# Optimization experiments

Measured on AMD Instinct MI355X. Metric: run time of the kernel, lower is better.

Reference implementation:

```python
import jax, jax.numpy as jnp
import numpy as np

N_NODES = 50000
N_EDGES = 800000
HIDDEN = 128
IN_DIM = 6
N_ACTIONS = 64
NUM_GRAPHS = 512


def setup_inputs() -> dict:
    key = jax.random.key(0)
    ks = jax.random.split(key, 9)
    x = jax.random.normal(ks[0], (N_NODES, IN_DIM), dtype=jnp.float32)
    edge_index = jax.random.randint(ks[1], (2, N_EDGES), 0, N_NODES, dtype=jnp.int64)
    batch_number = jnp.sort(jax.random.randint(ks[2], (N_NODES,), 0, NUM_GRAPHS, dtype=jnp.int64))
    s1 = 1.0 / np.sqrt(IN_DIM)
    s2 = 1.0 / np.sqrt(HIDDEN)
    w1 = jax.random.uniform(ks[3], (IN_DIM, HIDDEN), jnp.float32, -s1, s1)
    b1 = jnp.zeros((HIDDEN,), jnp.float32)
    wl = jax.random.uniform(ks[4], (HIDDEN, HIDDEN), jnp.float32, -s2, s2)
    bl = jax.random.uniform(ks[5], (HIDDEN,), jnp.float32, -s2, s2)
    w2 = jax.random.uniform(ks[6], (HIDDEN, N_ACTIONS), jnp.float32, -s2, s2)
    b2 = jax.random.uniform(ks[7], (N_ACTIONS,), jnp.float32, -s2, s2)
    return {"x": x, "edge_index": edge_index, "batch_number": batch_number,
            "w1": w1, "b1": b1, "wl": wl, "bl": bl, "w2": w2, "b2": b2}


def _gcn_conv(x, edge_index, w, b):
    # PyG GCNConv: add self-loops, symmetric D^-1/2 (A+I) D^-1/2, linear first.
    n = x.shape[0]
    loop = jnp.arange(n, dtype=edge_index.dtype)
    src = jnp.concatenate([edge_index[0], loop])
    dst = jnp.concatenate([edge_index[1], loop])
    deg = jax.ops.segment_sum(jnp.ones_like(dst, dtype=x.dtype), dst, num_segments=n)
    dinv = jax.lax.rsqrt(jnp.maximum(deg, 1.0))  # deg >= 1 from self-loops
    norm = dinv[src] * dinv[dst]                  # [E+N]
    h = x @ w                                     # [N, hidden]
    msg = h[src] * norm[:, None]                  # gather + edge-wise scale
    return jax.ops.segment_sum(msg, dst, num_segments=n) + b


def reference(x, edge_index, batch_number, w1, b1, wl, bl, w2, b2):
    h = jax.nn.relu(_gcn_conv(x, edge_index, w1, b1))          # [N, hidden]
    # scatter_mean over graphs in the batch
    gsum = jax.ops.segment_sum(h, batch_number, num_segments=NUM_GRAPHS)
    cnt = jax.ops.segment_sum(jnp.ones((h.shape[0],), h.dtype), batch_number,
                              num_segments=NUM_GRAPHS)
    g = gsum / jnp.maximum(cnt, 1.0)[:, None]                  # [G, hidden]
    g = jax.nn.relu(g @ wl + bl)
    logits = g @ w2 + b2                                       # [G, actions]
    return jax.nn.log_softmax(logits, axis=1)
```

## Files before the change

kernel.cpp:

```cpp
#include <hip/hip_runtime.h>
#include <math.h>

#define N_NODES 50000
#define N_EDGES 800000
#define HID     128
#define N_ACT   64
#define N_GRAPH 512
#define N6      (N_NODES * 6)

#define NWF    512
#define LOGW   9
#define WF     98
#define CB     8
#define DC     8
#define EPB    2048
#define PB     ((N_EDGES + EPB - 1) / EPB)
#define SEGCAP 64
#define SSH    6
#define MAXIT  7

#define MAXN  768

#define F_BUCKET 0
#define F_COUNTS (F_BUCKET + (WF * PB + 512) * SEGCAP)
#define F_GSTART (F_COUNTS + 38320)
#define F_DINV   (F_GSTART + 516)
#define F_XSPAD  (F_DINV + N_NODES)
#define F_DEGP   (F_XSPAD + N_NODES * 8)
#define F_SPART  (F_DEGP + DC * N_NODES)
#define F_TOTAL  (F_SPART + CB * N6)
#define NEED_BYTES ((size_t)F_TOTAL * 4)


__global__ __launch_bounds__(512) void k_place(const int* __restrict__ ei,
                                               int* __restrict__ bucket,
                                               int* __restrict__ counts) {
    __shared__ int lc[WF];
    int t = threadIdx.x;
    int b = blockIdx.x;
    if (t < WF) lc[t] = 0;
    __syncthreads();
    int e0 = b * EPB;
    int pk[4], wli[4];
#pragma unroll
    for (int i = 0; i < 4; ++i) {
        int e = e0 + i * 512 + t;
        wli[i] = -1;
        if (e < N_EDGES) {
            int src = ei[e], dst = ei[N_EDGES + e];
            int w = dst >> LOGW;
            int lp = atomicAdd(&lc[w], 1);
            pk[i] = ((dst - (w << LOGW)) << 16) | src;
            wli[i] = (w << 16) | lp;
        }
    }
    __syncthreads();
    if (t < WF) counts[t * PB + b] = min(lc[t], SEGCAP);
#pragma unroll
    for (int i = 0; i < 4; ++i) {
        if (wli[i] >= 0) {
            int w = wli[i] >> 16, lp = wli[i] & 0xffff;
            if (lp < SEGCAP) bucket[((w * PB + b) << SSH) + lp] = pk[i];
        }
    }
}

__global__ __launch_bounds__(512) void k_degp(const int* __restrict__ bucket,
                                              const int* __restrict__ counts,
                                              float* __restrict__ degp) {
    __shared__ float hist[NWF];
    __shared__ int scnt[64];
    int w = blockIdx.x, c = blockIdx.y;
    int t = threadIdx.x;
    int nseg = (PB - 1 - c) / DC + 1;
    if (t < NWF) hist[t] = 0.0f;
    if (t < 64) scnt[t] = 0;
    __syncthreads();
    if (t < nseg) scnt[t] = counts[w * PB + c + DC * t];
    __syncthreads();
    int base = (w * PB + c) << SSH;
    int pk[MAXIT];
    bool val[MAXIT];
#pragma unroll
    for (int i = 0; i < MAXIT; ++i) {
        int s = t + i * 512;
        int j = s >> SSH, e = s & (SEGCAP - 1);
        val[i] = e < scnt[j];
        pk[i] = bucket[base + ((j * DC) << SSH) + e];
    }
#pragma unroll
    for (int i = 0; i < MAXIT; ++i)
        if (val[i]) atomicAdd(&hist[((unsigned)pk[i]) >> 16], 1.0f);
    __syncthreads();
    int nb = w * NWF;
    int lim = min(NWF, N_NODES - nb);
    if (t < lim) degp[c * N_NODES + nb + t] = hist[t];
}

__device__ __forceinline__ void mark_gstart(const int* __restrict__ batch, int m,
                                            int* __restrict__ gstart) {
    int bm = batch[m];
    if (m == 0) {
        for (int g = 0; g <= bm; ++g) gstart[g] = 0;
    } else {
        int bp = batch[m - 1];
        for (int g = bp + 1; g <= bm; ++g) gstart[g] = m;
    }
    if (m == N_NODES - 1) {
        for (int g = bm + 1; g <= N_GRAPH; ++g) gstart[g] = N_NODES;
    }
}

__global__ __launch_bounds__(256) void k_scale2(const float* __restrict__ degp,
                                                const float* __restrict__ x,
                                                const int* __restrict__ batch,
                                                float* __restrict__ dinv,
                                                float* __restrict__ xs_pad,
                                                int* __restrict__ gstart) {
    int n = blockIdx.x * 512 + 2 * threadIdx.x;
    if (n >= N_NODES) return;
    float d0 = 1.0f, d1 = 1.0f;
#pragma unroll
    for (int c = 0; c < DC; ++c) {
        d0 += degp[c * N_NODES + n];
        d1 += degp[c * N_NODES + n + 1];
    }
    float dv0 = rsqrtf(d0), dv1 = rsqrtf(d1);
    dinv[n] = dv0; dinv[n + 1] = dv1;
    const float4* xp = (const float4*)(x + (size_t)n * 6);
    float4 xa = xp[0], xb = xp[1], xc = xp[2];
    float4* op = (float4*)(xs_pad + (size_t)n * 8);
    op[0] = make_float4(xa.x * dv0, xa.y * dv0, xa.z * dv0, xa.w * dv0);
    op[1] = make_float4(xb.x * dv0, xb.y * dv0, 0.0f, 0.0f);
    op[2] = make_float4(xb.z * dv1, xb.w * dv1, xc.x * dv1, xc.y * dv1);
    op[3] = make_float4(xc.z * dv1, xc.w * dv1, 0.0f, 0.0f);
    mark_gstart(batch, n, gstart);
    mark_gstart(batch, n + 1, gstart);
}

__global__ __launch_bounds__(512) void k_feat(const int* __restrict__ bucket,
                                              const int* __restrict__ counts,
                                              const float* __restrict__ xs_pad,
                                              float* __restrict__ s_part) {
    __shared__ float h[NWF * 6];
    __shared__ int scnt[64];
    int w = blockIdx.x, c = blockIdx.y;
    int t = threadIdx.x;
    float4* h4 = (float4*)h;
    for (int i = t; i < NWF * 6 / 4; i += 512) h4[i] = make_float4(0, 0, 0, 0);
    if (t < 64) scnt[t] = 0;
    __syncthreads();
    int nseg = (PB - 1 - c) / CB + 1;
    if (t < nseg) scnt[t] = counts[w * PB + c + CB * t];
    __syncthreads();
    int base = (w * PB + c) << SSH;

    int pk[MAXIT];
    bool val[MAXIT];
#pragma unroll
    for (int i = 0; i < MAXIT; ++i) {
        int s = t + i * 512;
        int j = s >> SSH, e = s & (SEGCAP - 1);
        val[i] = e < scnt[j];
        pk[i] = bucket[base + ((j * CB) << SSH) + e];
    }
    float4 ga[MAXIT], gb[MAXIT];
#pragma unroll
    for (int i = 0; i < MAXIT; ++i) {
        const float4* q = (const float4*)(xs_pad + (size_t)(pk[i] & 0xffff) * 8);
        ga[i] = q[0]; gb[i] = q[1];
    }
#pragma unroll
    for (int i = 0; i < MAXIT; ++i) {
        if (val[i]) {
            float* hp = &h[(((unsigned)pk[i]) >> 16) * 6];
            atomicAdd(hp + 0, ga[i].x); atomicAdd(hp + 1, ga[i].y); atomicAdd(hp + 2, ga[i].z);
            atomicAdd(hp + 3, ga[i].w); atomicAdd(hp + 4, gb[i].x); atomicAdd(hp + 5, gb[i].y);
        }
    }
    __syncthreads();
    int gbase = w * NWF * 6;
    int lim = min(NWF * 6, N6 - gbase);
    float4* sp4 = (float4*)(s_part + (size_t)c * N6 + gbase);
    for (int i = t; i < lim / 4; i += 512) sp4[i] = h4[i];
}

__global__ __launch_bounds__(512) void k_nodehead(const float* __restrict__ s_part,
                                                  const float* __restrict__ xs_pad,
                                                  const float* __restrict__ dinv,
                                                  const int* __restrict__ gstart,
                                                  const float* __restrict__ w1,
                                                  const float* __restrict__ b1,
                                                  const float* __restrict__ wl,
                                                  const float* __restrict__ bl,
                                                  const float* __restrict__ w2,
                                                  const float* __restrict__ b2,
                                                  float* __restrict__ out) {
    __shared__ float sb[MAXN * 6];
    __shared__ float dvb[MAXN];
    __shared__ float sg[4 * HID];
    __shared__ float sg2[4 * HID];
    __shared__ int gb[5];
    int t = threadIdx.x;
    int g0 = blockIdx.x * 4;
    if (t < 5) gb[t] = gstart[g0 + t];
    __syncthreads();
    int ns = gb[0], ne = gb[4];
    int sub = t >> 7, f = t & (HID - 1);
    float w1r[6];
#pragma unroll
    for (int k = 0; k < 6; ++k) w1r[k] = w1[k * HID + f];
    float b1f = b1[f];
    float acc = 0.0f;

    for (int base = ns; base < ne; base += MAXN) {
        int cc = min(MAXN, ne - base);
        __syncthreads();
        {
            float2* sb2 = (float2*)sb;
            int nel = cc * 3;
            int g2 = base * 3;
            for (int i = t; i < nel; i += 512) {
                float2 v = make_float2(0.0f, 0.0f);
#pragma unroll
                for (int c = 0; c < CB; ++c) {
                    float2 p = ((const float2*)(s_part + (size_t)c * N6))[g2 + i];
                    v.x += p.x; v.y += p.y;
                }
                sb2[i] = v;
            }
        }
        for (int i = t; i < cc; i += 512) {
            int n = base + i;
            const float4* xp = (const float4*)(xs_pad + (size_t)n * 8);
            float4 a = xp[0], bq = xp[1];
            float* sp = &sb[i * 6];
            sp[0] += a.x; sp[1] += a.y; sp[2] += a.z;
            sp[3] += a.w; sp[4] += bq.x; sp[5] += bq.y;
            dvb[i] = dinv[n];
        }
        __syncthreads();
        int lo = max(gb[sub], base);
        int hi = min(gb[sub + 1], base + cc);
        for (int n = lo; n < hi; ++n) {
            int i = n - base;
            const float* sp = &sb[i * 6];
            float tv = 0.0f;
#pragma unroll
            for (int k = 0; k < 6; ++k) tv = fmaf(sp[k], w1r[k], tv);
            acc += fmaxf(fmaf(dvb[i], tv, b1f), 0.0f);
        }
    }

    int cnt = gb[sub + 1] - gb[sub];
    float ic = 1.0f / fmaxf((float)cnt, 1.0f);
    sg[sub * HID + f] = acc * ic;
    __syncthreads();

    float a2 = bl[f];
    for (int k = 0; k < HID; ++k) a2 = fmaf(sg[sub * HID + k], wl[k * HID + f], a2);
    sg2[sub * HID + f] = fmaxf(a2, 0.0f);
    __syncthreads();

    if (f < N_ACT) {
        float l = b2[f];
        for (int ff = 0; ff < HID; ++ff) l = fmaf(sg2[sub * HID + ff], w2[ff * N_ACT + f], l);
        float m = l;
#pragma unroll
        for (int off = 32; off > 0; off >>= 1) m = fmaxf(m, __shfl_xor(m, off));
        float e = expf(l - m);
        float ssum = e;
#pragma unroll
        for (int off = 32; off > 0; off >>= 1) ssum += __shfl_xor(ssum, off);
        out[(g0 + sub) * N_ACT + f] = l - m - logf(ssum);
    }
}


__global__ void k_init(float* __restrict__ deg, float* __restrict__ gsum,
                       float* __restrict__ cnt) {
    int i = blockIdx.x * blockDim.x + threadIdx.x;
    if (i < N_NODES) deg[i] = 1.0f;
    if (i < N_GRAPH * HID) gsum[i] = 0.0f;
    if (i < N_GRAPH) cnt[i] = 0.0f;
}

__global__ void k_deg(const int* __restrict__ ei, float* __restrict__ deg) {
    int e = blockIdx.x * blockDim.x + threadIdx.x;
    if (e < N_EDGES) atomicAdd(&deg[ei[N_EDGES + e]], 1.0f);
}

__global__ void k_scale(const float* __restrict__ x, const int* __restrict__ batch,
                        const float* __restrict__ deg, float* __restrict__ dinv,
                        float* __restrict__ xs, float* __restrict__ s,
                        float* __restrict__ cnt) {
    int n = blockIdx.x * blockDim.x + threadIdx.x;
    if (n >= N_NODES) return;
    float dv = rsqrtf(deg[n]);
    dinv[n] = dv;
#pragma unroll
    for (int k = 0; k < 6; ++k) {
        float v = x[n * 6 + k] * dv;
        xs[n * 6 + k] = v;
        s[n * 6 + k] = v;
    }
    atomicAdd(&cnt[batch[n]], 1.0f);
}

__global__ void k_scatter(const int* __restrict__ ei, const float* __restrict__ xs,
                          float* __restrict__ s) {
    int e = blockIdx.x * blockDim.x + threadIdx.x;
    if (e >= N_EDGES) return;
    int src = ei[e];
    int dst = ei[N_EDGES + e];
#pragma unroll
    for (int k = 0; k < 6; ++k)
        atomicAdd(&s[dst * 6 + k], xs[src * 6 + k]);
}

__global__ __launch_bounds__(256) void k_node(const float* __restrict__ s,
                                              const float* __restrict__ dinv,
                                              const int* __restrict__ batch,
                                              const float* __restrict__ w1,
                                              const float* __restrict__ b1,
                                              float* __restrict__ gsum) {
    int f = threadIdx.x & (HID - 1);
    int sub = threadIdx.x >> 7;
    int base = blockIdx.x * 16 + sub * 8;
    float w1r[6];
#pragma unroll
    for (int k = 0; k < 6; ++k) w1r[k] = w1[k * HID + f];
    float b1f = b1[f];
    float acc = 0.0f;
    int curb = -1;
    for (int i = 0; i < 8; ++i) {
        int n = base + i;
        if (n >= N_NODES) break;
        float t = 0.0f;
#pragma unroll
        for (int k = 0; k < 6; ++k) t = fmaf(s[n * 6 + k], w1r[k], t);
        float a = fmaxf(fmaf(dinv[n], t, b1f), 0.0f);
        int b = batch[n];
        if (b != curb) {
            if (curb >= 0) atomicAdd(&gsum[curb * HID + f], acc);
            acc = 0.0f;
            curb = b;
        }
        acc += a;
    }
    if (curb >= 0) atomicAdd(&gsum[curb * HID + f], acc);
}

__global__ __launch_bounds__(128) void k_head(const float* __restrict__ gsum,
                                              const float* __restrict__ cnt,
                                              const float* __restrict__ wl,
                                              const float* __restrict__ bl,
                                              const float* __restrict__ w2,
                                              const float* __restrict__ b2,
                                              float* __restrict__ out) {
    __shared__ float sg[HID];
    __shared__ float sg2[HID];
    int g = blockIdx.x;
    int t = threadIdx.x;

    float ic = 1.0f / fmaxf(cnt[g], 1.0f);
    sg[t] = gsum[g * HID + t] * ic;
    __syncthreads();

    float acc = bl[t];
    for (int k = 0; k < HID; ++k) acc = fmaf(sg[k], wl[k * HID + t], acc);
    sg2[t] = fmaxf(acc, 0.0f);
    __syncthreads();

    if (t < N_ACT) {
        float l = b2[t];
        for (int f = 0; f < HID; ++f) l = fmaf(sg2[f], w2[f * N_ACT + t], l);
        float m = l;
#pragma unroll
        for (int off = 32; off > 0; off >>= 1) m = fmaxf(m, __shfl_xor(m, off));
        float e = expf(l - m);
        float ssum = e;
#pragma unroll
        for (int off = 32; off > 0; off >>= 1) ssum += __shfl_xor(ssum, off);
        out[g * N_ACT + t] = l - m - logf(ssum);
    }
}


extern "C" void kernel_launch(void* const* d_in, const int* in_sizes, int n_in,
                              void* d_out, int out_size, void* d_ws, size_t ws_size,
                              hipStream_t stream) {
    const float* x     = (const float*)d_in[0];
    const int*   ei    = (const int*)d_in[1];
    const int*   batch = (const int*)d_in[2];
    const float* w1    = (const float*)d_in[3];
    const float* b1    = (const float*)d_in[4];
    const float* wl    = (const float*)d_in[5];
    const float* bl    = (const float*)d_in[6];
    const float* w2    = (const float*)d_in[7];
    const float* b2    = (const float*)d_in[8];
    float* out = (float*)d_out;
    float* ws = (float*)d_ws;

    if (ws_size >= NEED_BYTES) {
        int*   bucket = (int*)(ws + F_BUCKET);
        int*   counts = (int*)(ws + F_COUNTS);
        int*   gstart = (int*)(ws + F_GSTART);
        float* dinv   = ws + F_DINV;
        float* xs_pad = ws + F_XSPAD;
        float* degp   = ws + F_DEGP;
        float* s_part = ws + F_SPART;

        k_place<<<PB, 512, 0, stream>>>(ei, bucket, counts);
        k_degp<<<dim3(WF, DC), 512, 0, stream>>>(bucket, counts, degp);
        k_scale2<<<(N_NODES + 511) / 512, 256, 0, stream>>>(degp, x, batch, dinv, xs_pad, gstart);
        k_feat<<<dim3(WF, CB), 512, 0, stream>>>(bucket, counts, xs_pad, s_part);
        k_nodehead<<<N_GRAPH / 4, 512, 0, stream>>>(s_part, xs_pad, dinv, gstart,
                                                    w1, b1, wl, bl, w2, b2, out);
    } else {
        float* deg  = ws;
        float* dinv = deg + N_NODES;
        float* xs   = dinv + N_NODES;
        float* s    = xs + N6;
        float* gsum = s + N6;
        float* cnt  = gsum + N_GRAPH * HID;

        k_init<<<(N_GRAPH * HID + 255) / 256, 256, 0, stream>>>(deg, gsum, cnt);
        k_deg<<<(N_EDGES + 255) / 256, 256, 0, stream>>>(ei, deg);
        k_scale<<<(N_NODES + 255) / 256, 256, 0, stream>>>(x, batch, deg, dinv, xs, s, cnt);
        k_scatter<<<(N_EDGES + 255) / 256, 256, 0, stream>>>(ei, xs, s);
        k_node<<<(N_NODES + 15) / 16, 256, 0, stream>>>(s, dinv, batch, w1, b1, gsum);
        k_head<<<N_GRAPH, 128, 0, stream>>>(gsum, cnt, wl, bl, w2, b2, out);
    }
}
```

Measured before the change: 79.41 us.

## Eliminate scale kernel by recomputing dinv on the fly from transposed degree partials

Removes the k_scale2 launch. The gstart marking moves into k_place, and k_degp writes its degree partials node-major (8 per node), so k_feat and k_nodehead can each sum them and take rsqrt per gathered source instead of reading a precomputed scaled-x buffer. This saves one kernel launch and the xs_pad/dinv round trip through memory. In exchange, every edge gathers 32 B of degree partials plus 24 B of x (via float2 loads) and runs an extra rsqrt, which raises gather traffic in k_feat.

```diff
diff --git a/kernel.cpp b/kernel.cpp
--- a/kernel.cpp
+++ b/kernel.cpp
@@ -24,22 +24,40 @@
 #define F_BUCKET 0
 #define F_COUNTS (F_BUCKET + (WF * PB + 512) * SEGCAP)
 #define F_GSTART (F_COUNTS + 38320)
-#define F_DINV   (F_GSTART + 516)
-#define F_XSPAD  (F_DINV + N_NODES)
-#define F_DEGP   (F_XSPAD + N_NODES * 8)
-#define F_SPART  (F_DEGP + DC * N_NODES)
+#define F_DEGPT  (F_GSTART + 516)
+#define F_SPART  (F_DEGPT + N_NODES * 8)
 #define F_TOTAL  (F_SPART + CB * N6)
 #define NEED_BYTES ((size_t)F_TOTAL * 4)
 
+__device__ __forceinline__ void mark_gstart(const int* __restrict__ batch, int m,
+                                            int* __restrict__ gstart) {
+    int bm = batch[m];
+    if (m == 0) {
+        for (int g = 0; g <= bm; ++g) gstart[g] = 0;
+    } else {
+        int bp = batch[m - 1];
+        for (int g = bp + 1; g <= bm; ++g) gstart[g] = m;
+    }
+    if (m == N_NODES - 1) {
+        for (int g = bm + 1; g <= N_GRAPH; ++g) gstart[g] = N_NODES;
+    }
+}
+
 
 __global__ __launch_bounds__(512) void k_place(const int* __restrict__ ei,
+                                               const int* __restrict__ batch,
                                                int* __restrict__ bucket,
-                                               int* __restrict__ counts) {
+                                               int* __restrict__ counts,
+                                               int* __restrict__ gstart) {
     __shared__ int lc[WF];
     int t = threadIdx.x;
     int b = blockIdx.x;
     if (t < WF) lc[t] = 0;
     __syncthreads();
+    {
+        int m = b * 128 + t;
+        if (t < 128 && m < N_NODES) mark_gstart(batch, m, gstart);
+    }
     int e0 = b * EPB;
     int pk[4], wli[4];
 #pragma unroll
@@ -67,7 +85,7 @@
 
 __global__ __launch_bounds__(512) void k_degp(const int* __restrict__ bucket,
                                               const int* __restrict__ counts,
-                                              float* __restrict__ degp) {
+                                              float* __restrict__ degpt) {
     __shared__ float hist[NWF];
     __shared__ int scnt[64];
     int w = blockIdx.x, c = blockIdx.y;
@@ -94,53 +112,13 @@
     __syncthreads();
     int nb = w * NWF;
     int lim = min(NWF, N_NODES - nb);
-    if (t < lim) degp[c * N_NODES + nb + t] = hist[t];
-}
-
-__device__ __forceinline__ void mark_gstart(const int* __restrict__ batch, int m,
-                                            int* __restrict__ gstart) {
-    int bm = batch[m];
-    if (m == 0) {
-        for (int g = 0; g <= bm; ++g) gstart[g] = 0;
-    } else {
-        int bp = batch[m - 1];
-        for (int g = bp + 1; g <= bm; ++g) gstart[g] = m;
-    }
-    if (m == N_NODES - 1) {
-        for (int g = bm + 1; g <= N_GRAPH; ++g) gstart[g] = N_NODES;
-    }
-}
-
-__global__ __launch_bounds__(256) void k_scale2(const float* __restrict__ degp,
-                                                const float* __restrict__ x,
-                                                const int* __restrict__ batch,
-                                                float* __restrict__ dinv,
-                                                float* __restrict__ xs_pad,
-                                                int* __restrict__ gstart) {
-    int n = blockIdx.x * 512 + 2 * threadIdx.x;
-    if (n >= N_NODES) return;
-    float d0 = 1.0f, d1 = 1.0f;
-#pragma unroll
-    for (int c = 0; c < DC; ++c) {
-        d0 += degp[c * N_NODES + n];
-        d1 += degp[c * N_NODES + n + 1];
-    }
-    float dv0 = rsqrtf(d0), dv1 = rsqrtf(d1);
-    dinv[n] = dv0; dinv[n + 1] = dv1;
-    const float4* xp = (const float4*)(x + (size_t)n * 6);
-    float4 xa = xp[0], xb = xp[1], xc = xp[2];
-    float4* op = (float4*)(xs_pad + (size_t)n * 8);
-    op[0] = make_float4(xa.x * dv0, xa.y * dv0, xa.z * dv0, xa.w * dv0);
-    op[1] = make_float4(xb.x * dv0, xb.y * dv0, 0.0f, 0.0f);
-    op[2] = make_float4(xb.z * dv1, xb.w * dv1, xc.x * dv1, xc.y * dv1);
-    op[3] = make_float4(xc.z * dv1, xc.w * dv1, 0.0f, 0.0f);
-    mark_gstart(batch, n, gstart);
-    mark_gstart(batch, n + 1, gstart);
+    if (t < lim) degpt[(size_t)(nb + t) * 8 + c] = hist[t];
 }
 
 __global__ __launch_bounds__(512) void k_feat(const int* __restrict__ bucket,
                                               const int* __restrict__ counts,
-                                              const float* __restrict__ xs_pad,
+                                              const float* __restrict__ degpt,
+                                              const float* __restrict__ x,
                                               float* __restrict__ s_part) {
     __shared__ float h[NWF * 6];
     __shared__ int scnt[64];
@@ -157,6 +135,7 @@
 
     int pk[MAXIT];
     bool val[MAXIT];
+    int sr[MAXIT];
 #pragma unroll
     for (int i = 0; i < MAXIT; ++i) {
         int s = t + i * 512;
@@ -164,18 +143,28 @@
         val[i] = e < scnt[j];
         pk[i] = bucket[base + ((j * CB) << SSH) + e];
     }
-    float4 ga[MAXIT], gb[MAXIT];
+#pragma unroll
+    for (int i = 0; i < MAXIT; ++i)
+        sr[i] = val[i] ? (pk[i] & 0xffff) : 0;
+    float4 da[MAXIT], db[MAXIT];
+    float2 xa[MAXIT], xbv[MAXIT], xcv[MAXIT];
 #pragma unroll
     for (int i = 0; i < MAXIT; ++i) {
-        const float4* q = (const float4*)(xs_pad + (size_t)(pk[i] & 0xffff) * 8);
-        ga[i] = q[0]; gb[i] = q[1];
+        const float4* dp = (const float4*)(degpt + (size_t)sr[i] * 8);
+        da[i] = dp[0]; db[i] = dp[1];
+        const float2* xp = (const float2*)(x + (size_t)sr[i] * 6);
+        xa[i] = xp[0]; xbv[i] = xp[1]; xcv[i] = xp[2];
     }
 #pragma unroll
     for (int i = 0; i < MAXIT; ++i) {
         if (val[i]) {
+            float d = 1.0f + da[i].x + da[i].y + da[i].z + da[i].w
+                           + db[i].x + db[i].y + db[i].z + db[i].w;
+            float dv = rsqrtf(d);
             float* hp = &h[(((unsigned)pk[i]) >> 16) * 6];
-            atomicAdd(hp + 0, ga[i].x); atomicAdd(hp + 1, ga[i].y); atomicAdd(hp + 2, ga[i].z);
-            atomicAdd(hp + 3, ga[i].w); atomicAdd(hp + 4, gb[i].x); atomicAdd(hp + 5, gb[i].y);
+            atomicAdd(hp + 0, xa[i].x * dv);  atomicAdd(hp + 1, xa[i].y * dv);
+            atomicAdd(hp + 2, xbv[i].x * dv); atomicAdd(hp + 3, xbv[i].y * dv);
+            atomicAdd(hp + 4, xcv[i].x * dv); atomicAdd(hp + 5, xcv[i].y * dv);
         }
     }
     __syncthreads();
@@ -186,8 +175,8 @@
 }
 
 __global__ __launch_bounds__(512) void k_nodehead(const float* __restrict__ s_part,
-                                                  const float* __restrict__ xs_pad,
-                                                  const float* __restrict__ dinv,
+                                                  const float* __restrict__ degpt,
+                                                  const float* __restrict__ x,
                                                   const int* __restrict__ gstart,
                                                   const float* __restrict__ w1,
                                                   const float* __restrict__ b1,
@@ -232,12 +221,16 @@
         }
         for (int i = t; i < cc; i += 512) {
             int n = base + i;
-            const float4* xp = (const float4*)(xs_pad + (size_t)n * 8);
-            float4 a = xp[0], bq = xp[1];
+            const float4* dp = (const float4*)(degpt + (size_t)n * 8);
+            float4 da = dp[0], db = dp[1];
+            float d = 1.0f + da.x + da.y + da.z + da.w + db.x + db.y + db.z + db.w;
+            float dv = rsqrtf(d);
+            dvb[i] = dv;
+            const float2* xp = (const float2*)(x + (size_t)n * 6);
+            float2 x0 = xp[0], x1 = xp[1], x2 = xp[2];
             float* sp = &sb[i * 6];
-            sp[0] += a.x; sp[1] += a.y; sp[2] += a.z;
-            sp[3] += a.w; sp[4] += bq.x; sp[5] += bq.y;
-            dvb[i] = dinv[n];
+            sp[0] += x0.x * dv; sp[1] += x0.y * dv; sp[2] += x1.x * dv;
+            sp[3] += x1.y * dv; sp[4] += x2.x * dv; sp[5] += x2.y * dv;
         }
         __syncthreads();
         int lo = max(gb[sub], base);
@@ -406,16 +399,13 @@
         int*   bucket = (int*)(ws + F_BUCKET);
         int*   counts = (int*)(ws + F_COUNTS);
         int*   gstart = (int*)(ws + F_GSTART);
-        float* dinv   = ws + F_DINV;
-        float* xs_pad = ws + F_XSPAD;
-        float* degp   = ws + F_DEGP;
+        float* degpt  = ws + F_DEGPT;
         float* s_part = ws + F_SPART;
 
-        k_place<<<PB, 512, 0, stream>>>(ei, bucket, counts);
-        k_degp<<<dim3(WF, DC), 512, 0, stream>>>(bucket, counts, degp);
-        k_scale2<<<(N_NODES + 511) / 512, 256, 0, stream>>>(degp, x, batch, dinv, xs_pad, gstart);
-        k_feat<<<dim3(WF, CB), 512, 0, stream>>>(bucket, counts, xs_pad, s_part);
-        k_nodehead<<<N_GRAPH / 4, 512, 0, stream>>>(s_part, xs_pad, dinv, gstart,
+        k_place<<<PB, 512, 0, stream>>>(ei, batch, bucket, counts, gstart);
+        k_degp<<<dim3(WF, DC), 512, 0, stream>>>(bucket, counts, degpt);
+        k_feat<<<dim3(WF, CB), 512, 0, stream>>>(bucket, counts, degpt, x, s_part);
+        k_nodehead<<<N_GRAPH / 4, 512, 0, stream>>>(s_part, degpt, x, gstart,
                                                     w1, b1, wl, bl, w2, b2, out);
     } else {
         float* deg  = ws;
```

Result: no change. 80.97 us (+2.0%).
